# Optimization experiments

Hardware: AMD Instinct MI355X
Metric: run time of the kernel (lower is better)

Reference implementation:

```python
import jax, jax.numpy as jnp
import numpy as np

B, N, S = 16, 4096, 1024
D1, D2 = 128, 256          # points1 / points2 channel dims
IN_CH, OUT_CH = D1 + D2, 128
EPS_BN = 1e-5


def setup_inputs() -> dict:
    key = jax.random.key(0)
    ks = jax.random.split(key, 16)
    inp = {
        "xyz1": jax.random.normal(ks[0], (B, N, 3), jnp.float32),
        "xyz2": jax.random.normal(ks[1], (B, S, 3), jnp.float32),
        "points1": jax.random.normal(ks[2], (B, D1, N), jnp.float32),
        "points2": jax.random.normal(ks[3], (B, D2, S), jnp.float32),
        # fuse: 1x1 Conv (IN_CH -> OUT_CH) + BN + ReLU
        "fuse_w": jax.random.normal(ks[4], (OUT_CH, IN_CH), jnp.float32) * 0.05,
        "fuse_b": jnp.zeros((OUT_CH,), jnp.float32),
        "fuse_g": jnp.ones((OUT_CH,), jnp.float32),
        "fuse_be": jnp.zeros((OUT_CH,), jnp.float32),
        # extraction: 1 residual pointwise block (res_expansion=1.0)
        "w1": jax.random.normal(ks[5], (OUT_CH, OUT_CH), jnp.float32) * 0.05,
        "b1": jnp.zeros((OUT_CH,), jnp.float32),
        "g1": jnp.ones((OUT_CH,), jnp.float32),
        "be1": jnp.zeros((OUT_CH,), jnp.float32),
        "w2": jax.random.normal(ks[6], (OUT_CH, OUT_CH), jnp.float32) * 0.05,
        "b2": jnp.zeros((OUT_CH,), jnp.float32),
        "g2": jnp.ones((OUT_CH,), jnp.float32),
        "be2": jnp.zeros((OUT_CH,), jnp.float32),
    }
    return inp


def _bn(x, gamma, beta):
    # train-mode batchnorm over (batch, point) dims; x: [B, N, C]
    mu = jnp.mean(x, axis=(0, 1), keepdims=True)
    var = jnp.var(x, axis=(0, 1), keepdims=True)
    return (x - mu) * jax.lax.rsqrt(var + EPS_BN) * gamma + beta


def reference(xyz1, xyz2, points1, points2,
              fuse_w, fuse_b, fuse_g, fuse_be,
              w1, b1, g1, be1, w2, b2, g2, be2):
    # points2 -> [B, S, D2]
    p2 = jnp.transpose(points2, (0, 2, 1))
    # squared pairwise distances [B, N, S]
    d = (jnp.sum(xyz1 * xyz1, -1)[:, :, None]
         + jnp.sum(xyz2 * xyz2, -1)[:, None, :]
         - 2.0 * jnp.einsum("bnc,bsc->bns", xyz1, xyz2))
    # 3 nearest neighbors (equiv to full sort + [:, :, :3])
    neg_d3, idx = jax.lax.top_k(-d, 3)          # [B, N, 3]
    d3 = -neg_d3
    recip = 1.0 / (d3 + 1e-8)
    weight = recip / jnp.sum(recip, axis=2, keepdims=True)  # [B, N, 3]
    gathered = p2[jnp.arange(B)[:, None, None], idx]        # [B, N, 3, D2]
    interp = jnp.sum(gathered * weight[..., None], axis=2)  # [B, N, D2]
    # concat skip features: [B, N, D1+D2]
    feats = jnp.concatenate([jnp.transpose(points1, (0, 2, 1)), interp], axis=-1)
    # fuse: 1x1 conv + BN + ReLU
    x = jnp.einsum("bnc,oc->bno", feats, fuse_w) + fuse_b
    x = jax.nn.relu(_bn(x, fuse_g, fuse_be))
    # extraction: residual pointwise block
    h = jnp.einsum("bnc,oc->bno", x, w1) + b1
    h = jax.nn.relu(_bn(h, g1, be1))
    h = jnp.einsum("bnc,oc->bno", h, w2) + b2
    h = _bn(h, g2, be2)
    out = jax.nn.relu(h + x)
    return jnp.transpose(out, (0, 2, 1))  # [B, OUT_CH, N]
```

## Files before the change

kernel.cpp:

```cpp
#include <hip/hip_runtime.h>

#define BB   16
#define NN   4096
#define SS   1024
#define D1C  128
#define D2C  256
#define CIN  384
#define CO   128
#define MM   (BB*NN)

typedef __attribute__((ext_vector_type(8))) short short8;
typedef __attribute__((ext_vector_type(8))) unsigned short ushort8;
typedef __attribute__((ext_vector_type(4))) float f32x4;

__device__ __forceinline__ unsigned short f2bf(float f) {
  unsigned u = __builtin_bit_cast(unsigned, f);
  u += 0x7fffu + ((u >> 16) & 1u);
  return (unsigned short)(u >> 16);
}
__device__ __forceinline__ float bf2f(unsigned short u) {
  unsigned x = ((unsigned)u) << 16;
  return __builtin_bit_cast(float, x);
}

__global__ __launch_bounds__(64) void arrange_all(
    const float* __restrict__ w0, const float* __restrict__ w1, const float* __restrict__ w2,
    uint4* __restrict__ wf0, uint4* __restrict__ wf1, uint4* __restrict__ wf2) {
  int blk = blockIdx.x;
  const float* w; uint4* wf; int K; int local;
  if (blk < 96)       { w = w0; wf = wf0; K = CIN; local = blk; }
  else if (blk < 128) { w = w1; wf = wf1; K = CO;  local = blk - 96; }
  else                { w = w2; wf = wf2; K = CO;  local = blk - 128; }
  int lane = threadIdx.x;
  int id = local * 64 + lane;
  int ob = (id >> 6) & 7;
  int kt = id >> 9;
  int o = ob * 16 + (lane & 15);
  int k = kt * 32 + (lane >> 4) * 8;
  const float* src = w + (size_t)o * K + k;
  union { unsigned short u[8]; uint4 v; } p;
  #pragma unroll
  for (int j = 0; j < 8; ++j) p.u[j] = f2bf(src[j]);
  wf[id] = p.v;
}

__global__ __launch_bounds__(256) void transp2(const float* __restrict__ p2,
                                               unsigned short* __restrict__ p2t) {
  int b  = blockIdx.x >> 6;
  int s0 = (blockIdx.x & 63) * 16;
  int c  = threadIdx.x;
  const float* src = p2 + ((size_t)b * D2C + c) * SS + s0;
  float v[16];
  #pragma unroll
  for (int k = 0; k < 4; ++k) {
    float4 x = *(const float4*)(src + k * 4);
    v[k*4+0] = x.x; v[k*4+1] = x.y; v[k*4+2] = x.z; v[k*4+3] = x.w;
  }
  unsigned short* dst = p2t + ((size_t)b * SS + s0) * D2C + c;
  #pragma unroll
  for (int s = 0; s < 16; ++s) dst[(size_t)s * D2C] = f2bf(v[s]);
}

#define INS(dd, ii) { if ((dd) < d2) { if ((dd) < d1) { if ((dd) < d0) { \
  d2=d1;i2=i1; d1=d0;i1=i0; d0=(dd);i0=(ii); } else { d2=d1;i2=i1; d1=(dd);i1=(ii); } } \
  else { d2=(dd);i2=(ii); } } }

__global__ __launch_bounds__(256) void top3_kernel(const float* __restrict__ xyz1,
                                                   const float* __restrict__ xyz2,
                                                   int* __restrict__ idx3,
                                                   float* __restrict__ w3) {
  __shared__ float4 sp[SS];
  int b  = blockIdx.x >> 6;
  int nb = (blockIdx.x & 63) * 64;
  int t  = threadIdx.x;
  const float* x2 = xyz2 + (size_t)b * SS * 3;
  for (int i = t; i < SS; i += 256) {
    float a = x2[i*3+0], c = x2[i*3+1], d = x2[i*3+2];
    sp[i] = make_float4(a, c, d, a*a + c*c + d*d);
  }
  __syncthreads();
  int nl = t >> 2, q = t & 3;
  int n  = nb + nl;
  size_t gm = (size_t)b * NN + n;
  float px = xyz1[gm*3+0], py = xyz1[gm*3+1], pz = xyz1[gm*3+2];
  float n1 = px*px + py*py + pz*pz;
  float d0 = 3.4e38f, d1 = 3.4e38f, d2 = 3.4e38f;
  int   i0 = 0, i1 = 0, i2 = 0;
  int sbase = q * 256;
  #pragma unroll 4
  for (int s = 0; s < 256; ++s) {
    float4 p = sp[sbase + s];
    float d = n1 + p.w - 2.0f * (px*p.x + py*p.y + pz*p.z);
    INS(d, sbase + s);
  }
  #pragma unroll
  for (int msk = 1; msk <= 2; msk <<= 1) {
    float e0 = __shfl_xor(d0, msk), e1 = __shfl_xor(d1, msk), e2 = __shfl_xor(d2, msk);
    int   j0 = __shfl_xor(i0, msk), j1 = __shfl_xor(i1, msk), j2 = __shfl_xor(i2, msk);
    INS(e0, j0); INS(e1, j1); INS(e2, j2);
  }
  if (q == 0) {
    float r0 = 1.0f/(d0 + 1e-8f), r1 = 1.0f/(d1 + 1e-8f), r2 = 1.0f/(d2 + 1e-8f);
    float inv = 1.0f/(r0 + r1 + r2);
    idx3[gm*3+0] = i0; idx3[gm*3+1] = i1; idx3[gm*3+2] = i2;
    w3  [gm*3+0] = r0*inv; w3[gm*3+1] = r1*inv; w3[gm*3+2] = r2*inv;
  }
}

__global__ __launch_bounds__(256, 4) void gemm1_mfma(
    const float* __restrict__ p1, const unsigned short* __restrict__ p2t,
    const int* __restrict__ idx3, const float* __restrict__ w3,
    const uint4* __restrict__ wfrag, const float* __restrict__ bias,
    unsigned short* __restrict__ outb, float* __restrict__ pblk) {
  __shared__ float sSum[128], sSsq[128];
  int t = threadIdx.x;
  int wid = t >> 6, lane = t & 63;
  if (t < 128) { sSum[t] = 0.f; sSsq[t] = 0.f; }
  int bid = blockIdx.x;
  bid = (bid & 7) * 128 + (bid >> 3);
  int m0 = bid * 64 + wid * 16;
  int b  = m0 >> 12;
  int cl = lane & 15, g = lane >> 4;
  int m  = m0 + cl;
  int n  = m & (NN - 1);
  int i0 = idx3[(size_t)m*3+0], i1 = idx3[(size_t)m*3+1], i2 = idx3[(size_t)m*3+2];
  float wA = w3[(size_t)m*3+0], wB = w3[(size_t)m*3+1], wC = w3[(size_t)m*3+2];
  const unsigned short* r0 = p2t + ((size_t)b * SS + i0) * D2C;
  const unsigned short* r1 = p2t + ((size_t)b * SS + i1) * D2C;
  const unsigned short* r2 = p2t + ((size_t)b * SS + i2) * D2C;
  const float* p1b = p1 + (size_t)b * D1C * NN + n;
  f32x4 acc[8] = {};
  for (int kt = 0; kt < 12; ++kt) {
    short8 bv;
    if (kt < 4) {
      int kbase = kt * 32 + g * 8;
      #pragma unroll
      for (int j = 0; j < 8; ++j) bv[j] = (short)f2bf(p1b[(size_t)(kbase + j) * NN]);
    } else {
      int c0 = (kt - 4) * 32 + g * 8;
      ushort8 u0 = *(const ushort8*)(r0 + c0);
      ushort8 u1 = *(const ushort8*)(r1 + c0);
      ushort8 u2 = *(const ushort8*)(r2 + c0);
      #pragma unroll
      for (int j = 0; j < 8; ++j)
        bv[j] = (short)f2bf(wA*bf2f(u0[j]) + wB*bf2f(u1[j]) + wC*bf2f(u2[j]));
    }
    const uint4* wk = wfrag + (size_t)kt * 512 + lane;
    #pragma unroll
    for (int ob = 0; ob < 8; ++ob) {
      short8 av = __builtin_bit_cast(short8, wk[ob * 64]);
      acc[ob] = __builtin_amdgcn_mfma_f32_16x16x32_bf16(av, bv, acc[ob], 0, 0, 0);
    }
  }
  __syncthreads();
  #pragma unroll
  for (int ob = 0; ob < 8; ++ob) {
    #pragma unroll
    for (int r = 0; r < 4; ++r) {
      int o = ob * 16 + g * 4 + r;
      float v = acc[ob][r] + bias[o];
      outb[(size_t)o * MM + m] = f2bf(v);
      float s = v, q = v * v;
      #pragma unroll
      for (int off = 1; off < 16; off <<= 1) { s += __shfl_xor(s, off); q += __shfl_xor(q, off); }
      if (cl == 0) { atomicAdd(&sSum[o], s); atomicAdd(&sSsq[o], q); }
    }
  }
  __syncthreads();
  if (t < 128) {
    pblk[(size_t)blockIdx.x * 256 + t]       = sSum[t];
    pblk[(size_t)blockIdx.x * 256 + 128 + t] = sSsq[t];
  }
}

__global__ __launch_bounds__(256, 4) void gemm23_mfma(
    const unsigned short* __restrict__ inb, const float* __restrict__ scale,
    const float* __restrict__ shift, const uint4* __restrict__ wfrag,
    const float* __restrict__ bias, unsigned short* __restrict__ outb,
    float* __restrict__ pblk) {
  __shared__ float sSum[128], sSsq[128];
  int t = threadIdx.x;
  int wid = t >> 6, lane = t & 63;
  if (t < 128) { sSum[t] = 0.f; sSsq[t] = 0.f; }
  int bid = blockIdx.x;
  bid = (bid & 7) * 128 + (bid >> 3);
  int m0 = bid * 64 + wid * 16;
  int cl = lane & 15, g = lane >> 4;
  int m  = m0 + cl;
  const unsigned short* src = inb + m;
  f32x4 acc[8] = {};
  for (int kt = 0; kt < 4; ++kt) {
    int kbase = kt * 32 + g * 8;
    short8 bv;
    #pragma unroll
    for (int j = 0; j < 8; ++j) {
      int c = kbase + j;
      float x = bf2f(src[(size_t)c * MM]);
      bv[j] = (short)f2bf(fmaxf(fmaf(x, scale[c], shift[c]), 0.f));
    }
    const uint4* wk = wfrag + (size_t)kt * 512 + lane;
    #pragma unroll
    for (int ob = 0; ob < 8; ++ob) {
      short8 av = __builtin_bit_cast(short8, wk[ob * 64]);
      acc[ob] = __builtin_amdgcn_mfma_f32_16x16x32_bf16(av, bv, acc[ob], 0, 0, 0);
    }
  }
  __syncthreads();
  #pragma unroll
  for (int ob = 0; ob < 8; ++ob) {
    #pragma unroll
    for (int r = 0; r < 4; ++r) {
      int o = ob * 16 + g * 4 + r;
      float v = acc[ob][r] + bias[o];
      outb[(size_t)o * MM + m] = f2bf(v);
      float s = v, q = v * v;
      #pragma unroll
      for (int off = 1; off < 16; off <<= 1) { s += __shfl_xor(s, off); q += __shfl_xor(q, off); }
      if (cl == 0) { atomicAdd(&sSum[o], s); atomicAdd(&sSsq[o], q); }
    }
  }
  __syncthreads();
  if (t < 128) {
    pblk[(size_t)blockIdx.x * 256 + t]       = sSum[t];
    pblk[(size_t)blockIdx.x * 256 + 128 + t] = sSsq[t];
  }
}

__global__ __launch_bounds__(256) void reduce_fin(const float* __restrict__ pblk,
                                                  const float* __restrict__ g,
                                                  const float* __restrict__ be,
                                                  float* __restrict__ scale,
                                                  float* __restrict__ shift) {
  int o = blockIdx.x, t = threadIdx.x;
  float s = 0.f, q = 0.f;
  #pragma unroll
  for (int it = 0; it < 4; ++it) {
    const float* p = pblk + (size_t)(it * 256 + t) * 256;
    s += p[o]; q += p[128 + o];
  }
  #pragma unroll
  for (int off = 32; off; off >>= 1) { s += __shfl_down(s, off, 64); q += __shfl_down(q, off, 64); }
  __shared__ float ls[4], lq[4];
  if ((t & 63) == 0) { ls[t >> 6] = s; lq[t >> 6] = q; }
  __syncthreads();
  if (t == 0) {
    float S = ls[0]+ls[1]+ls[2]+ls[3], Q = lq[0]+lq[1]+lq[2]+lq[3];
    const float invM = 1.0f / (float)MM;
    float mean = S * invM;
    float var  = Q * invM - mean * mean;
    float rstd = rsqrtf(var + 1e-5f);
    float sc   = g[o] * rstd;
    scale[o] = sc;
    shift[o] = fmaf(-mean, sc, be[o]);
  }
}

__global__ __launch_bounds__(256) void final_kernel(
    const unsigned short* __restrict__ bufX, const unsigned short* __restrict__ bufH2,
    const float* __restrict__ bnp, float* __restrict__ out) {
  int lin = blockIdx.x * 256 + threadIdx.x;
  int o = lin >> 13;
  int r = lin & 8191;
  int m = r * 8;
  int b = m >> 12;
  int n = m & (NN - 1);
  float s0 = bnp[o], t0 = bnp[128 + o], s2 = bnp[512 + o], t2 = bnp[640 + o];
  ushort8 xu = *(const ushort8*)(bufX  + (size_t)o * MM + m);
  ushort8 hu = *(const ushort8*)(bufH2 + (size_t)o * MM + m);
  float y[8];
  #pragma unroll
  for (int j = 0; j < 8; ++j) {
    float x = bf2f(xu[j]), h = bf2f(hu[j]);
    y[j] = fmaxf(fmaf(h, s2, t2) + fmaxf(fmaf(x, s0, t0), 0.f), 0.f);
  }
  float* dst = out + (size_t)b * CO * NN + (size_t)o * NN + n;
  *(float4*)dst       = make_float4(y[0], y[1], y[2], y[3]);
  *(float4*)(dst + 4) = make_float4(y[4], y[5], y[6], y[7]);
}

extern "C" void kernel_launch(void* const* d_in, const int* in_sizes, int n_in,
                              void* d_out, int out_size, void* d_ws, size_t ws_size,
                              hipStream_t stream) {
  const float* xyz1    = (const float*)d_in[0];
  const float* xyz2    = (const float*)d_in[1];
  const float* points1 = (const float*)d_in[2];
  const float* points2 = (const float*)d_in[3];
  const float* fuse_w  = (const float*)d_in[4];
  const float* fuse_b  = (const float*)d_in[5];
  const float* fuse_g  = (const float*)d_in[6];
  const float* fuse_be = (const float*)d_in[7];
  const float* w1      = (const float*)d_in[8];
  const float* b1      = (const float*)d_in[9];
  const float* g1      = (const float*)d_in[10];
  const float* be1     = (const float*)d_in[11];
  const float* w2      = (const float*)d_in[12];
  const float* b2      = (const float*)d_in[13];
  const float* g2      = (const float*)d_in[14];
  const float* be2     = (const float*)d_in[15];

  char* ws = (char*)d_ws;
  size_t off = 0;
  auto alloc = [&](size_t bytes) -> void* {
    void* p = ws + off;
    off += (bytes + 255) & ~(size_t)255;
    return p;
  };
  int*            idx3 = (int*)           alloc((size_t)MM * 3 * 4);
  float*          w3   = (float*)         alloc((size_t)MM * 3 * 4);
  uint4*          wf0  = (uint4*)         alloc((size_t)96 * 64 * 16);
  uint4*          wf1  = (uint4*)         alloc((size_t)32 * 64 * 16);
  uint4*          wf2  = (uint4*)         alloc((size_t)32 * 64 * 16);
  float*          pblk = (float*)         alloc((size_t)1024 * 256 * 4);
  float*          bnp  = (float*)         alloc(6 * 128 * 4);
  unsigned short* p2t  = (unsigned short*)alloc((size_t)BB * SS * D2C * 2);
  unsigned short* bufX = (unsigned short*)alloc((size_t)MM * CO * 2);
  unsigned short* bufH = (unsigned short*)alloc((size_t)MM * CO * 2);
  unsigned short* bufH2= (unsigned short*)alloc((size_t)MM * CO * 2);
  if (off > ws_size) return;

  arrange_all<<<160, 64, 0, stream>>>(fuse_w, w1, w2, wf0, wf1, wf2);
  transp2<<<BB * 64, 256, 0, stream>>>(points2, p2t);
  top3_kernel<<<BB * 64, 256, 0, stream>>>(xyz1, xyz2, idx3, w3);

  gemm1_mfma<<<MM/64, 256, 0, stream>>>(points1, p2t, idx3, w3, wf0, fuse_b, bufX, pblk);
  reduce_fin<<<128, 256, 0, stream>>>(pblk, fuse_g, fuse_be, bnp + 0, bnp + 128);

  gemm23_mfma<<<MM/64, 256, 0, stream>>>(bufX, bnp + 0, bnp + 128, wf1, b1, bufH, pblk);
  reduce_fin<<<128, 256, 0, stream>>>(pblk, g1, be1, bnp + 256, bnp + 384);

  gemm23_mfma<<<MM/64, 256, 0, stream>>>(bufH, bnp + 256, bnp + 384, wf2, b2, bufH2, pblk);
  reduce_fin<<<128, 256, 0, stream>>>(pblk, g2, be2, bnp + 512, bnp + 640);

  final_kernel<<<(CO * (MM/8)) / 256, 256, 0, stream>>>(bufX, bufH2, bnp, (float*)d_out);
}
```

Baseline: 299.0 us.

## Switch intermediate activations to point-major layout with LDS-staged epilogue

Intermediate bf16 buffers change from channel-major [C][M] to point-major [M][C], so each GEMM lane reads contiguous 16-byte channel vectors instead of strided scalar loads. points1 is pre-transposed into bf16 by a new kernel. The epilogue is rewritten to stage the output tile in LDS, write coalesced 16-byte rows, and compute BN partial sums by column reduction instead of shuffles plus shared atomics. Gather loads are issued early, packed bf16 conversion is used, and the final kernel transposes through LDS back to [B,C,N]. This costs an extra transpose pass over points1 and more LDS per block.

```diff
diff --git a/kernel.cpp b/kernel.cpp
--- a/kernel.cpp
+++ b/kernel.cpp
@@ -21,6 +21,14 @@
 __device__ __forceinline__ float bf2f(unsigned short u) {
   unsigned x = ((unsigned)u) << 16;
   return __builtin_bit_cast(float, x);
+}
+__device__ __forceinline__ unsigned cvt_pk(float lo, float hi) {
+  unsigned r;
+  asm("v_cvt_pk_bf16_f32 %0, %1, %2" : "=v"(r) : "v"(lo), "v"(hi));
+  return r;
+}
+__device__ __forceinline__ ushort8 ld8(const unsigned short* p) {
+  return *(const ushort8*)p;
 }
 
 __global__ __launch_bounds__(64) void arrange_all(
@@ -61,6 +69,25 @@
   for (int s = 0; s < 16; ++s) dst[(size_t)s * D2C] = f2bf(v[s]);
 }
 
+__global__ __launch_bounds__(256) void transp1(const float* __restrict__ p1,
+                                               unsigned short* __restrict__ p1t) {
+  int b  = blockIdx.x >> 7;
+  int n0 = (blockIdx.x & 127) * 32;
+  int c  = threadIdx.x & 127;
+  int nh = threadIdx.x >> 7;
+  int n  = n0 + nh * 16;
+  const float* src = p1 + ((size_t)b * D1C + c) * NN + n;
+  float v[16];
+  #pragma unroll
+  for (int k = 0; k < 4; ++k) {
+    float4 x = *(const float4*)(src + k * 4);
+    v[k*4+0] = x.x; v[k*4+1] = x.y; v[k*4+2] = x.z; v[k*4+3] = x.w;
+  }
+  unsigned short* dst = p1t + ((size_t)b * NN + n) * D1C + c;
+  #pragma unroll
+  for (int s = 0; s < 16; ++s) dst[(size_t)s * D1C] = f2bf(v[s]);
+}
+
 #define INS(dd, ii) { if ((dd) < d2) { if ((dd) < d1) { if ((dd) < d0) { \
   d2=d1;i2=i1; d1=d0;i1=i0; d0=(dd);i0=(ii); } else { d2=d1;i2=i1; d1=(dd);i1=(ii); } } \
   else { d2=(dd);i2=(ii); } } }
@@ -107,70 +134,122 @@
   }
 }
 
+__device__ __forceinline__ void gemm_epilogue(
+    f32x4 acc[8], const float* __restrict__ bias,
+    unsigned short* __restrict__ outb, float* __restrict__ pblk,
+    int m0b, int wid, int cl, int g, int t, int rawblk) {
+  __shared__ unsigned short tile[64][136];
+  __shared__ float sS[256], sQ[256];
+  #pragma unroll
+  for (int ob = 0; ob < 8; ++ob) {
+    float4 bs = *(const float4*)(bias + ob * 16 + g * 4);
+    float v0 = acc[ob][0] + bs.x, v1 = acc[ob][1] + bs.y;
+    float v2 = acc[ob][2] + bs.z, v3 = acc[ob][3] + bs.w;
+    uint2 pk;
+    pk.x = cvt_pk(v0, v1);
+    pk.y = cvt_pk(v2, v3);
+    *(uint2*)&tile[wid * 16 + cl][ob * 16 + g * 4] = pk;
+  }
+  __syncthreads();
+  int c = t & 127, half = t >> 7;
+  float s = 0.f, q = 0.f;
+  #pragma unroll
+  for (int i = 0; i < 32; ++i) {
+    float v = bf2f(tile[half * 32 + i][c]);
+    s += v; q = fmaf(v, v, q);
+  }
+  sS[t] = s; sQ[t] = q;
+  int m_l = t >> 2, cq = (t & 3) * 32;
+  unsigned short* gdst = outb + (size_t)(m0b + m_l) * CO + cq;
+  #pragma unroll
+  for (int qd = 0; qd < 4; ++qd)
+    *(uint4*)(gdst + qd * 8) = *(const uint4*)&tile[m_l][cq + qd * 8];
+  __syncthreads();
+  if (t < 128) {
+    pblk[(size_t)rawblk * 256 + t]       = sS[t] + sS[t + 128];
+    pblk[(size_t)rawblk * 256 + 128 + t] = sQ[t] + sQ[t + 128];
+  }
+}
+
 __global__ __launch_bounds__(256, 4) void gemm1_mfma(
-    const float* __restrict__ p1, const unsigned short* __restrict__ p2t,
+    const unsigned short* __restrict__ p1t, const unsigned short* __restrict__ p2t,
     const int* __restrict__ idx3, const float* __restrict__ w3,
     const uint4* __restrict__ wfrag, const float* __restrict__ bias,
     unsigned short* __restrict__ outb, float* __restrict__ pblk) {
-  __shared__ float sSum[128], sSsq[128];
   int t = threadIdx.x;
   int wid = t >> 6, lane = t & 63;
-  if (t < 128) { sSum[t] = 0.f; sSsq[t] = 0.f; }
-  int bid = blockIdx.x;
-  bid = (bid & 7) * 128 + (bid >> 3);
-  int m0 = bid * 64 + wid * 16;
+  int rawblk = blockIdx.x;
+  int bid = (rawblk & 7) * 128 + (rawblk >> 3);
+  int m0b = bid * 64;
+  int m0 = m0b + wid * 16;
   int b  = m0 >> 12;
   int cl = lane & 15, g = lane >> 4;
   int m  = m0 + cl;
-  int n  = m & (NN - 1);
   int i0 = idx3[(size_t)m*3+0], i1 = idx3[(size_t)m*3+1], i2 = idx3[(size_t)m*3+2];
   float wA = w3[(size_t)m*3+0], wB = w3[(size_t)m*3+1], wC = w3[(size_t)m*3+2];
-  const unsigned short* r0 = p2t + ((size_t)b * SS + i0) * D2C;
-  const unsigned short* r1 = p2t + ((size_t)b * SS + i1) * D2C;
-  const unsigned short* r2 = p2t + ((size_t)b * SS + i2) * D2C;
-  const float* p1b = p1 + (size_t)b * D1C * NN + n;
+  const unsigned short* r0 = p2t + ((size_t)b * SS + i0) * D2C + g * 8;
+  const unsigned short* r1 = p2t + ((size_t)b * SS + i1) * D2C + g * 8;
+  const unsigned short* r2 = p2t + ((size_t)b * SS + i2) * D2C + g * 8;
+  const unsigned short* pr = p1t + (size_t)m * D1C + g * 8;
+
+  ushort8 pt[4], ua[4][3];
+  #pragma unroll
+  for (int kt = 0; kt < 4; ++kt) pt[kt] = ld8(pr + kt * 32);
+  #pragma unroll
+  for (int q = 0; q < 4; ++q) {
+    int c0 = q * 32;
+    ua[q][0] = ld8(r0 + c0); ua[q][1] = ld8(r1 + c0); ua[q][2] = ld8(r2 + c0);
+  }
   f32x4 acc[8] = {};
-  for (int kt = 0; kt < 12; ++kt) {
-    short8 bv;
-    if (kt < 4) {
-      int kbase = kt * 32 + g * 8;
-      #pragma unroll
-      for (int j = 0; j < 8; ++j) bv[j] = (short)f2bf(p1b[(size_t)(kbase + j) * NN]);
-    } else {
-      int c0 = (kt - 4) * 32 + g * 8;
-      ushort8 u0 = *(const ushort8*)(r0 + c0);
-      ushort8 u1 = *(const ushort8*)(r1 + c0);
-      ushort8 u2 = *(const ushort8*)(r2 + c0);
-      #pragma unroll
-      for (int j = 0; j < 8; ++j)
-        bv[j] = (short)f2bf(wA*bf2f(u0[j]) + wB*bf2f(u1[j]) + wC*bf2f(u2[j]));
-    }
+  #pragma unroll
+  for (int kt = 0; kt < 4; ++kt) {
+    short8 bv = __builtin_bit_cast(short8, pt[kt]);
     const uint4* wk = wfrag + (size_t)kt * 512 + lane;
     #pragma unroll
-    for (int ob = 0; ob < 8; ++ob) {
-      short8 av = __builtin_bit_cast(short8, wk[ob * 64]);
-      acc[ob] = __builtin_amdgcn_mfma_f32_16x16x32_bf16(av, bv, acc[ob], 0, 0, 0);
-    }
-  }
-  __syncthreads();
-  #pragma unroll
-  for (int ob = 0; ob < 8; ++ob) {
-    #pragma unroll
-    for (int r = 0; r < 4; ++r) {
-      int o = ob * 16 + g * 4 + r;
-      float v = acc[ob][r] + bias[o];
-      outb[(size_t)o * MM + m] = f2bf(v);
-      float s = v, q = v * v;
-      #pragma unroll
-      for (int off = 1; off < 16; off <<= 1) { s += __shfl_xor(s, off); q += __shfl_xor(q, off); }
-      if (cl == 0) { atomicAdd(&sSum[o], s); atomicAdd(&sSsq[o], q); }
-    }
-  }
-  __syncthreads();
-  if (t < 128) {
-    pblk[(size_t)blockIdx.x * 256 + t]       = sSum[t];
-    pblk[(size_t)blockIdx.x * 256 + 128 + t] = sSsq[t];
-  }
+    for (int ob = 0; ob < 8; ++ob)
+      acc[ob] = __builtin_amdgcn_mfma_f32_16x16x32_bf16(
+          __builtin_bit_cast(short8, wk[ob * 64]), bv, acc[ob], 0, 0, 0);
+  }
+  #pragma unroll
+  for (int q = 0; q < 4; ++q) {
+    float f[8];
+    #pragma unroll
+    for (int j = 0; j < 8; ++j)
+      f[j] = wA*bf2f(ua[q][0][j]) + wB*bf2f(ua[q][1][j]) + wC*bf2f(ua[q][2][j]);
+    uint4 pk;
+    pk.x = cvt_pk(f[0], f[1]); pk.y = cvt_pk(f[2], f[3]);
+    pk.z = cvt_pk(f[4], f[5]); pk.w = cvt_pk(f[6], f[7]);
+    short8 bv = __builtin_bit_cast(short8, pk);
+    const uint4* wk = wfrag + (size_t)(4 + q) * 512 + lane;
+    #pragma unroll
+    for (int ob = 0; ob < 8; ++ob)
+      acc[ob] = __builtin_amdgcn_mfma_f32_16x16x32_bf16(
+          __builtin_bit_cast(short8, wk[ob * 64]), bv, acc[ob], 0, 0, 0);
+  }
+  __builtin_amdgcn_sched_barrier(0);
+  ushort8 ub[4][3];
+  #pragma unroll
+  for (int q = 0; q < 4; ++q) {
+    int c0 = 128 + q * 32;
+    ub[q][0] = ld8(r0 + c0); ub[q][1] = ld8(r1 + c0); ub[q][2] = ld8(r2 + c0);
+  }
+  #pragma unroll
+  for (int q = 0; q < 4; ++q) {
+    float f[8];
+    #pragma unroll
+    for (int j = 0; j < 8; ++j)
+      f[j] = wA*bf2f(ub[q][0][j]) + wB*bf2f(ub[q][1][j]) + wC*bf2f(ub[q][2][j]);
+    uint4 pk;
+    pk.x = cvt_pk(f[0], f[1]); pk.y = cvt_pk(f[2], f[3]);
+    pk.z = cvt_pk(f[4], f[5]); pk.w = cvt_pk(f[6], f[7]);
+    short8 bv = __builtin_bit_cast(short8, pk);
+    const uint4* wk = wfrag + (size_t)(8 + q) * 512 + lane;
+    #pragma unroll
+    for (int ob = 0; ob < 8; ++ob)
+      acc[ob] = __builtin_amdgcn_mfma_f32_16x16x32_bf16(
+          __builtin_bit_cast(short8, wk[ob * 64]), bv, acc[ob], 0, 0, 0);
+  }
+  gemm_epilogue(acc, bias, outb, pblk, m0b, wid, cl, g, t, rawblk);
 }
 
 __global__ __launch_bounds__(256, 4) void gemm23_mfma(
@@ -178,52 +257,44 @@
     const float* __restrict__ shift, const uint4* __restrict__ wfrag,
     const float* __restrict__ bias, unsigned short* __restrict__ outb,
     float* __restrict__ pblk) {
-  __shared__ float sSum[128], sSsq[128];
   int t = threadIdx.x;
   int wid = t >> 6, lane = t & 63;
-  if (t < 128) { sSum[t] = 0.f; sSsq[t] = 0.f; }
-  int bid = blockIdx.x;
-  bid = (bid & 7) * 128 + (bid >> 3);
-  int m0 = bid * 64 + wid * 16;
+  int rawblk = blockIdx.x;
+  int bid = (rawblk & 7) * 128 + (rawblk >> 3);
+  int m0b = bid * 64;
+  int m0 = m0b + wid * 16;
   int cl = lane & 15, g = lane >> 4;
   int m  = m0 + cl;
-  const unsigned short* src = inb + m;
+  const unsigned short* src = inb + (size_t)m * CO + g * 8;
+  ushort8 xv[4];
+  #pragma unroll
+  for (int kt = 0; kt < 4; ++kt) xv[kt] = ld8(src + kt * 32);
   f32x4 acc[8] = {};
+  #pragma unroll
   for (int kt = 0; kt < 4; ++kt) {
-    int kbase = kt * 32 + g * 8;
-    short8 bv;
-    #pragma unroll
-    for (int j = 0; j < 8; ++j) {
-      int c = kbase + j;
-      float x = bf2f(src[(size_t)c * MM]);
-      bv[j] = (short)f2bf(fmaxf(fmaf(x, scale[c], shift[c]), 0.f));
-    }
+    int kb = kt * 32 + g * 8;
+    float4 sa = *(const float4*)(scale + kb), sb = *(const float4*)(scale + kb + 4);
+    float4 ha = *(const float4*)(shift + kb), hb = *(const float4*)(shift + kb + 4);
+    float f[8];
+    f[0] = fmaxf(fmaf(bf2f(xv[kt][0]), sa.x, ha.x), 0.f);
+    f[1] = fmaxf(fmaf(bf2f(xv[kt][1]), sa.y, ha.y), 0.f);
+    f[2] = fmaxf(fmaf(bf2f(xv[kt][2]), sa.z, ha.z), 0.f);
+    f[3] = fmaxf(fmaf(bf2f(xv[kt][3]), sa.w, ha.w), 0.f);
+    f[4] = fmaxf(fmaf(bf2f(xv[kt][4]), sb.x, hb.x), 0.f);
+    f[5] = fmaxf(fmaf(bf2f(xv[kt][5]), sb.y, hb.y), 0.f);
+    f[6] = fmaxf(fmaf(bf2f(xv[kt][6]), sb.z, hb.z), 0.f);
+    f[7] = fmaxf(fmaf(bf2f(xv[kt][7]), sb.w, hb.w), 0.f);
+    uint4 pk;
+    pk.x = cvt_pk(f[0], f[1]); pk.y = cvt_pk(f[2], f[3]);
+    pk.z = cvt_pk(f[4], f[5]); pk.w = cvt_pk(f[6], f[7]);
+    short8 bv = __builtin_bit_cast(short8, pk);
     const uint4* wk = wfrag + (size_t)kt * 512 + lane;
     #pragma unroll
-    for (int ob = 0; ob < 8; ++ob) {
-      short8 av = __builtin_bit_cast(short8, wk[ob * 64]);
-      acc[ob] = __builtin_amdgcn_mfma_f32_16x16x32_bf16(av, bv, acc[ob], 0, 0, 0);
-    }
-  }
-  __syncthreads();
-  #pragma unroll
-  for (int ob = 0; ob < 8; ++ob) {
-    #pragma unroll
-    for (int r = 0; r < 4; ++r) {
-      int o = ob * 16 + g * 4 + r;
-      float v = acc[ob][r] + bias[o];
-      outb[(size_t)o * MM + m] = f2bf(v);
-      float s = v, q = v * v;
-      #pragma unroll
-      for (int off = 1; off < 16; off <<= 1) { s += __shfl_xor(s, off); q += __shfl_xor(q, off); }
-      if (cl == 0) { atomicAdd(&sSum[o], s); atomicAdd(&sSsq[o], q); }
-    }
-  }
-  __syncthreads();
-  if (t < 128) {
-    pblk[(size_t)blockIdx.x * 256 + t]       = sSum[t];
-    pblk[(size_t)blockIdx.x * 256 + 128 + t] = sSsq[t];
-  }
+    for (int ob = 0; ob < 8; ++ob)
+      acc[ob] = __builtin_amdgcn_mfma_f32_16x16x32_bf16(
+          __builtin_bit_cast(short8, wk[ob * 64]), bv, acc[ob], 0, 0, 0);
+  }
+  gemm_epilogue(acc, bias, outb, pblk, m0b, wid, cl, g, t, rawblk);
 }
 
 __global__ __launch_bounds__(256) void reduce_fin(const float* __restrict__ pblk,
@@ -258,24 +329,41 @@
 __global__ __launch_bounds__(256) void final_kernel(
     const unsigned short* __restrict__ bufX, const unsigned short* __restrict__ bufH2,
     const float* __restrict__ bnp, float* __restrict__ out) {
-  int lin = blockIdx.x * 256 + threadIdx.x;
-  int o = lin >> 13;
-  int r = lin & 8191;
-  int m = r * 8;
-  int b = m >> 12;
-  int n = m & (NN - 1);
-  float s0 = bnp[o], t0 = bnp[128 + o], s2 = bnp[512 + o], t2 = bnp[640 + o];
-  ushort8 xu = *(const ushort8*)(bufX  + (size_t)o * MM + m);
-  ushort8 hu = *(const ushort8*)(bufH2 + (size_t)o * MM + m);
-  float y[8];
-  #pragma unroll
-  for (int j = 0; j < 8; ++j) {
-    float x = bf2f(xu[j]), h = bf2f(hu[j]);
-    y[j] = fmaxf(fmaf(h, s2, t2) + fmaxf(fmaf(x, s0, t0), 0.f), 0.f);
-  }
-  float* dst = out + (size_t)b * CO * NN + (size_t)o * NN + n;
-  *(float4*)dst       = make_float4(y[0], y[1], y[2], y[3]);
-  *(float4*)(dst + 4) = make_float4(y[4], y[5], y[6], y[7]);
+  __shared__ float yt[128][33];
+  __shared__ float sb[512];
+  int t = threadIdx.x;
+  if (t < 128) {
+    sb[t]       = bnp[t];
+    sb[128 + t] = bnp[128 + t];
+    sb[256 + t] = bnp[512 + t];
+    sb[384 + t] = bnp[640 + t];
+  }
+  __syncthreads();
+  int m0 = blockIdx.x * 32;
+  int b  = m0 >> 12;
+  int n0 = m0 & (NN - 1);
+  int m_l = t >> 3;
+  int cq  = (t & 7) * 16;
+  size_t base = (size_t)(m0 + m_l) * CO + cq;
+  ushort8 xu0 = ld8(bufX  + base), xu1 = ld8(bufX  + base + 8);
+  ushort8 hu0 = ld8(bufH2 + base), hu1 = ld8(bufH2 + base + 8);
+  #pragma unroll
+  for (int j = 0; j < 16; ++j) {
+    int c = cq + j;
+    float x = bf2f(j < 8 ? xu0[j & 7] : xu1[j & 7]);
+    float h = bf2f(j < 8 ? hu0[j & 7] : hu1[j & 7]);
+    float y = fmaxf(fmaf(h, sb[256 + c], sb[384 + c]) +
+                    fmaxf(fmaf(x, sb[c], sb[128 + c]), 0.f), 0.f);
+    yt[c][m_l] = y;
+  }
+  __syncthreads();
+  int o  = t >> 1;
+  int nh = (t & 1) * 16;
+  float* dst = out + (size_t)b * CO * NN + (size_t)o * NN + n0 + nh;
+  #pragma unroll
+  for (int qd = 0; qd < 4; ++qd)
+    *(float4*)(dst + qd * 4) = make_float4(yt[o][nh + qd*4 + 0], yt[o][nh + qd*4 + 1],
+                                           yt[o][nh + qd*4 + 2], yt[o][nh + qd*4 + 3]);
 }
 
 extern "C" void kernel_launch(void* const* d_in, const int* in_sizes, int n_in,
@@ -313,6 +401,7 @@
   float*          pblk = (float*)         alloc((size_t)1024 * 256 * 4);
   float*          bnp  = (float*)         alloc(6 * 128 * 4);
   unsigned short* p2t  = (unsigned short*)alloc((size_t)BB * SS * D2C * 2);
+  unsigned short* p1t  = (unsigned short*)alloc((size_t)MM * D1C * 2);
   unsigned short* bufX = (unsigned short*)alloc((size_t)MM * CO * 2);
   unsigned short* bufH = (unsigned short*)alloc((size_t)MM * CO * 2);
   unsigned short* bufH2= (unsigned short*)alloc((size_t)MM * CO * 2);
@@ -320,9 +409,10 @@
 
   arrange_all<<<160, 64, 0, stream>>>(fuse_w, w1, w2, wf0, wf1, wf2);
   transp2<<<BB * 64, 256, 0, stream>>>(points2, p2t);
+  transp1<<<BB * 128, 256, 0, stream>>>(points1, p1t);
   top3_kernel<<<BB * 64, 256, 0, stream>>>(xyz1, xyz2, idx3, w3);
 
-  gemm1_mfma<<<MM/64, 256, 0, stream>>>(points1, p2t, idx3, w3, wf0, fuse_b, bufX, pblk);
+  gemm1_mfma<<<MM/64, 256, 0, stream>>>(p1t, p2t, idx3, w3, wf0, fuse_b, bufX, pblk);
   reduce_fin<<<128, 256, 0, stream>>>(pblk, fuse_g, fuse_be, bnp + 0, bnp + 128);
 
   gemm23_mfma<<<MM/64, 256, 0, stream>>>(bufX, bnp + 0, bnp + 128, wf1, b1, bufH, pblk);
@@ -331,5 +421,5 @@
   gemm23_mfma<<<MM/64, 256, 0, stream>>>(bufH, bnp + 256, bnp + 384, wf2, b2, bufH2, pblk);
   reduce_fin<<<128, 256, 0, stream>>>(pblk, g2, be2, bnp + 512, bnp + 640);
 
-  final_kernel<<<(CO * (MM/8)) / 256, 256, 0, stream>>>(bufX, bufH2, bnp, (float*)d_out);
-}
+  final_kernel<<<MM/32, 256, 0, stream>>>(bufX, bufH2, bnp, (float*)d_out);
+}
```

New measurement: 272.8 us. -8.8%, faster.
